# Performance work log

Hardware: AMD Instinct MI355X
Metric: run time of the kernel (lower is better)

## Reference

```python
import jax, jax.numpy as jnp
import numpy as np

K_PRED = 6
SCORE_TEMP = 0.5
MPA_THRESH = (2.5, 1.0, 2.0)   # meters, [veh, ped, cyc]
MTR_THRESH = (2.5, 1.0, 2.0)
TRACK_FUTURE = 91 - 11          # step_gt - step_current = 80


def setup_inputs() -> dict:
    key = jax.random.key(0)
    k1, k2, k3 = jax.random.split(key, 3)
    n_sc, n_ag, n_jf, n_step = 64, 64, 32, 80
    # scale 2.0 so endpoint pair distances straddle the ~2.5m NMS thresholds
    trajs = jax.random.normal(k1, (n_sc, n_jf, n_ag, n_step, 3), dtype=jnp.float32) * 2.0
    scores = jax.random.normal(k2, (n_sc, n_jf, n_ag), dtype=jnp.float32)
    ag_idx = jax.random.randint(k3, (n_sc, n_ag), 0, 3)
    ag_type = jax.nn.one_hot(ag_idx, 3, dtype=jnp.float32)  # [n_sc, n_ag, 3] one-hot
    return {"ag_type": ag_type, "trajs": trajs, "scores": scores}


def _type_thresh(ag_type, thresh_list):
    # ag_type [S,A,3] one-hot -> per-agent threshold [S,A]
    return ag_type @ jnp.asarray(thresh_list, dtype=ag_type.dtype)


def _endpoint_within(trajs, thresh):
    # use_ade=False: pairwise distance of final-step xy. trajs [S,A,J,T,3]
    end_xy = trajs[:, :, :, -1, :2]  # [S,A,J,2]
    d = jnp.linalg.norm(end_xy[:, :, :, None, :] - end_xy[:, :, None, :, :], axis=-1)
    return d < thresh[:, :, None, None]  # [S,A,J,J] bool


def _mtr_nms(trajs, scores, within, k_pred):
    # greedy: pick argmax, down-weight nearby modes by 0.01, kill picked with -1
    def step(sc, _):
        idx = jnp.argmax(sc, axis=-1)  # [S,A]
        w = jnp.take_along_axis(within, idx[:, :, None, None], axis=2)[:, :, 0]  # [S,A,J]
        sc = sc * ((~w).astype(sc.dtype) * 0.99 + 0.01)
        sc = jnp.where(jax.nn.one_hot(idx, sc.shape[-1], dtype=bool), -1.0, sc)
        return sc, idx

    _, idxs = jax.lax.scan(step, scores, None, length=k_pred)
    mode_idx = jnp.moveaxis(idxs, 0, -1)  # [S,A,k_pred]
    trajs_k = jnp.take_along_axis(trajs, mode_idx[:, :, :, None, None], axis=2)
    scores_k = jnp.take_along_axis(scores, mode_idx, axis=2)
    return trajs_k, scores_k / scores_k.sum(-1, keepdims=True)


def _mpa_nms_agent(scores, within):
    # scores [K], within [K,K]; visit modes in descending original-score order,
    # suppress mode k to 0.001 if any currently-higher-scoring mode is within thresh.
    order = jnp.argsort(-scores)

    def step(sc, k):
        mask = within[k] & (sc > sc[k])
        return sc.at[k].set(jnp.where(mask.any(), 0.001, sc[k])), None

    sc, _ = jax.lax.scan(step, scores, order)
    return sc


def reference(ag_type, trajs, scores):
    trajs = jnp.swapaxes(trajs, 1, 2)  # [S,A,J,T,3]
    scores = jax.nn.softmax(jnp.swapaxes(scores, 1, 2), axis=-1)  # [S,A,J]

    # mtr_nms: reduce n_joint_future -> k_pred (mtr_nms_thresh non-empty, aggr empty)
    within = _endpoint_within(trajs, _type_thresh(ag_type, MTR_THRESH))
    trajs, scores = _mtr_nms(trajs, scores, within, K_PRED)

    # mpa_nms: rescore the k_pred modes
    within = _endpoint_within(trajs, _type_thresh(ag_type, MPA_THRESH))
    scores = jax.vmap(jax.vmap(_mpa_nms_agent))(scores, within)
    scores = scores / scores.sum(-1, keepdims=True)

    # score temperature > 0
    scores = jax.nn.softmax(jnp.log(scores) / SCORE_TEMP, axis=-1)

    # downsample to 2Hz: [S,A,k_pred,16,3]
    return trajs[:, :, :, 4:TRACK_FUTURE:5], scores
```

## Files before the change

kernel.cpp:

```cpp
#include <hip/hip_runtime.h>


#define NSC 64
#define NAG 64
#define NJF 32
#define NSTEP 80
#define KP 6
#define TOUT 16

struct F3 { float x, y, z; };

__global__ __launch_bounds__(64)
void womd_pp2(const float* __restrict__ ag_type,
              const float* __restrict__ trajs,
              const float* __restrict__ scores,
              float* __restrict__ out)
{
    const int tid  = threadIdx.x;
    const int half = tid >> 5;
    const int hl   = tid & 31;
    const int s    = blockIdx.x >> 5;
    const int p    = blockIdx.x & 31;
    const int a    = p * 2 + half;

    __shared__ float exs[2][NJF][2];
    __shared__ float sms[2][NJF];
    __shared__ int   selsh[2][KP];

    float raw = scores[((size_t)s * NJF + hl) * NAG + a];
    size_t eoff = (((size_t)(s * NJF + hl) * NAG + a) * NSTEP + (NSTEP - 1)) * 3;
    float exx = trajs[eoff];
    float exy = trajs[eoff + 1];
    const float* at = ag_type + (size_t)(s * NAG + a) * 3;
    const float thresh = at[0] * 2.5f + at[1] * 1.0f + at[2] * 2.0f;

    exs[half][hl][0] = exx;
    exs[half][hl][1] = exy;

    float mx = raw;
    #pragma unroll
    for (int off = 16; off > 0; off >>= 1)
        mx = fmaxf(mx, __shfl_xor(mx, off, 32));
    float ev = expf(raw - mx);
    float sum = ev;
    #pragma unroll
    for (int off = 16; off > 0; off >>= 1)
        sum += __shfl_xor(sum, off, 32);
    float sm = ev / sum;
    sms[half][hl] = sm;

    __syncthreads();

    unsigned m = 0;
    #pragma unroll 8
    for (int j = 0; j < NJF; ++j) {
        float dx = exx - exs[half][j][0];
        float dy = exy - exs[half][j][1];
        if (sqrtf(dx * dx + dy * dy) < thresh) m |= (1u << j);
    }

    float ls = sm;
    #pragma unroll
    for (int k = 0; k < KP; ++k) {
        float v = ls; int idx = hl;
        #pragma unroll
        for (int off = 16; off > 0; off >>= 1) {
            float ov = __shfl_xor(v, off, 32);
            int   oi = __shfl_xor(idx, off, 32);
            if (ov > v || (ov == v && oi < idx)) { v = ov; idx = oi; }
        }
        unsigned wb = __shfl(m, idx, 32);
        ls *= ((wb >> hl) & 1u) ? 0.01f : 1.0f;
        if (hl == idx) ls = -1.0f;
        if (hl == 0) selsh[half][k] = idx;
    }
    __syncthreads();

    F3 pt[3];
    #pragma unroll
    for (int i = 0; i < 3; ++i) {
        int e  = hl + 32 * i;
        int mm = e >> 4;
        int t  = e & 15;
        int sj = selsh[half][mm];
        size_t src = (((size_t)(s * NJF + sj) * NAG + a) * NSTEP + (4 + 5 * t)) * 3;
        pt[i] = *(const F3*)(trajs + src);
    }

    if (hl == 0) {
        int   sel[KP];
        float sk[KP], sx[KP], sy[KP];
        float ssum = 0.f;
        #pragma unroll
        for (int k = 0; k < KP; ++k) {
            sel[k] = selsh[half][k];
            sk[k]  = sms[half][sel[k]];
            ssum  += sk[k];
            sx[k]  = exs[half][sel[k]][0];
            sy[k]  = exs[half][sel[k]][1];
        }
        #pragma unroll
        for (int k = 0; k < KP; ++k) sk[k] /= ssum;

        bool w2[KP][KP];
        #pragma unroll
        for (int i = 0; i < KP; ++i)
            #pragma unroll
            for (int j = 0; j < KP; ++j) {
                float dx = sx[i] - sx[j], dy = sy[i] - sy[j];
                w2[i][j] = sqrtf(dx * dx + dy * dy) < thresh;
            }

        int order[KP]; bool used[KP] = {false,false,false,false,false,false};
        #pragma unroll
        for (int t = 0; t < KP; ++t) {
            int best = -1; float bv = 0.f;
            #pragma unroll
            for (int j = 0; j < KP; ++j)
                if (!used[j] && (best < 0 || sk[j] > bv)) { best = j; bv = sk[j]; }
            order[t] = best; used[best] = true;
        }
        #pragma unroll
        for (int t = 0; t < KP; ++t) {
            int k = order[t];
            bool any = false;
            #pragma unroll
            for (int j = 0; j < KP; ++j)
                if (w2[k][j] && sk[j] > sk[k]) any = true;
            if (any) sk[k] = 0.001f;
        }

        float s2 = 0.f;
        #pragma unroll
        for (int k = 0; k < KP; ++k) s2 += sk[k];
        #pragma unroll
        for (int k = 0; k < KP; ++k) sk[k] /= s2;
        float s3 = 0.f; float q[KP];
        #pragma unroll
        for (int k = 0; k < KP; ++k) { q[k] = sk[k] * sk[k]; s3 += q[k]; }

        const size_t SCBASE = (size_t)NSC * NAG * KP * TOUT * 3;
        size_t scb = SCBASE + ((size_t)s * NAG + a) * KP;
        #pragma unroll
        for (int k = 0; k < KP; ++k) out[scb + k] = q[k] / s3;
    }

    size_t ob = ((size_t)s * NAG + a) * (KP * TOUT * 3);
    #pragma unroll
    for (int i = 0; i < 3; ++i) {
        int e = hl + 32 * i;
        *(F3*)(out + ob + (size_t)e * 3) = pt[i];
    }
}

extern "C" void kernel_launch(void* const* d_in, const int* in_sizes, int n_in,
                              void* d_out, int out_size, void* d_ws, size_t ws_size,
                              hipStream_t stream) {
    const float* ag_type = (const float*)d_in[0];
    const float* trajs   = (const float*)d_in[1];
    const float* scores  = (const float*)d_in[2];
    float* out = (float*)d_out;

    womd_pp2<<<NSC * (NAG / 2), 64, 0, stream>>>(ag_type, trajs, scores, out);
}
```

Before: 32.98 us.

## Parallelize MPA NMS across lanes and drop second block barrier

```diff
diff --git a/kernel.cpp b/kernel.cpp
--- a/kernel.cpp
+++ b/kernel.cpp
@@ -11,7 +11,7 @@
 struct F3 { float x, y, z; };
 
 __global__ __launch_bounds__(64)
-void womd_pp2(const float* __restrict__ ag_type,
+void womd_pp3(const float* __restrict__ ag_type,
               const float* __restrict__ trajs,
               const float* __restrict__ scores,
               float* __restrict__ out)
@@ -24,8 +24,6 @@
     const int a    = p * 2 + half;
 
     __shared__ float exs[2][NJF][2];
-    __shared__ float sms[2][NJF];
-    __shared__ int   selsh[2][KP];
 
     float raw = scores[((size_t)s * NJF + hl) * NAG + a];
     size_t eoff = (((size_t)(s * NJF + hl) * NAG + a) * NSTEP + (NSTEP - 1)) * 3;
@@ -47,18 +45,18 @@
     for (int off = 16; off > 0; off >>= 1)
         sum += __shfl_xor(sum, off, 32);
     float sm = ev / sum;
-    sms[half][hl] = sm;
 
     __syncthreads();
 
     unsigned m = 0;
-    #pragma unroll 8
+    #pragma unroll
     for (int j = 0; j < NJF; ++j) {
         float dx = exx - exs[half][j][0];
         float dy = exy - exs[half][j][1];
-        if (sqrtf(dx * dx + dy * dy) < thresh) m |= (1u << j);
+        m |= (sqrtf(dx * dx + dy * dy) < thresh) ? (1u << j) : 0u;
     }
 
+    int sel[KP];
     float ls = sm;
     #pragma unroll
     for (int k = 0; k < KP; ++k) {
@@ -67,89 +65,86 @@
         for (int off = 16; off > 0; off >>= 1) {
             float ov = __shfl_xor(v, off, 32);
             int   oi = __shfl_xor(idx, off, 32);
-            if (ov > v || (ov == v && oi < idx)) { v = ov; idx = oi; }
+            bool take = (ov > v) || (ov == v && oi < idx);
+            v   = take ? ov : v;
+            idx = take ? oi : idx;
         }
+        sel[k] = idx;
         unsigned wb = __shfl(m, idx, 32);
         ls *= ((wb >> hl) & 1u) ? 0.01f : 1.0f;
-        if (hl == idx) ls = -1.0f;
-        if (hl == 0) selsh[half][k] = idx;
+        ls = (hl == idx) ? -1.0f : ls;
     }
-    __syncthreads();
 
     F3 pt[3];
     #pragma unroll
     for (int i = 0; i < 3; ++i) {
-        int e  = hl + 32 * i;
-        int mm = e >> 4;
-        int t  = e & 15;
-        int sj = selsh[half][mm];
-        size_t src = (((size_t)(s * NJF + sj) * NAG + a) * NSTEP + (4 + 5 * t)) * 3;
+        int mode = (hl < 16) ? sel[2 * i] : sel[2 * i + 1];
+        int t = hl & 15;
+        size_t src = (((size_t)(s * NJF + mode) * NAG + a) * NSTEP + (4 + 5 * t)) * 3;
         pt[i] = *(const F3*)(trajs + src);
     }
 
-    if (hl == 0) {
-        int   sel[KP];
-        float sk[KP], sx[KP], sy[KP];
-        float ssum = 0.f;
-        #pragma unroll
-        for (int k = 0; k < KP; ++k) {
-            sel[k] = selsh[half][k];
-            sk[k]  = sms[half][sel[k]];
-            ssum  += sk[k];
-            sx[k]  = exs[half][sel[k]][0];
-            sy[k]  = exs[half][sel[k]][1];
-        }
-        #pragma unroll
-        for (int k = 0; k < KP; ++k) sk[k] /= ssum;
+    const bool active = (hl < KP);
+    int mySel = sel[0];
+    mySel = (hl == 1) ? sel[1] : mySel;
+    mySel = (hl == 2) ? sel[2] : mySel;
+    mySel = (hl == 3) ? sel[3] : mySel;
+    mySel = (hl == 4) ? sel[4] : mySel;
+    mySel = (hl == 5) ? sel[5] : mySel;
 
-        bool w2[KP][KP];
-        #pragma unroll
-        for (int i = 0; i < KP; ++i)
-            #pragma unroll
-            for (int j = 0; j < KP; ++j) {
-                float dx = sx[i] - sx[j], dy = sy[i] - sy[j];
-                w2[i][j] = sqrtf(dx * dx + dy * dy) < thresh;
-            }
+    float mySk = __shfl(sm, mySel, 32);
+    float myX  = __shfl(exx, mySel, 32);
+    float myY  = __shfl(exy, mySel, 32);
 
-        int order[KP]; bool used[KP] = {false,false,false,false,false,false};
-        #pragma unroll
-        for (int t = 0; t < KP; ++t) {
-            int best = -1; float bv = 0.f;
-            #pragma unroll
-            for (int j = 0; j < KP; ++j)
-                if (!used[j] && (best < 0 || sk[j] > bv)) { best = j; bv = sk[j]; }
-            order[t] = best; used[best] = true;
-        }
-        #pragma unroll
-        for (int t = 0; t < KP; ++t) {
-            int k = order[t];
-            bool any = false;
-            #pragma unroll
-            for (int j = 0; j < KP; ++j)
-                if (w2[k][j] && sk[j] > sk[k]) any = true;
-            if (any) sk[k] = 0.001f;
-        }
+    float t0 = active ? mySk : 0.f;
+    t0 += __shfl_xor(t0, 4, 8);
+    t0 += __shfl_xor(t0, 2, 8);
+    t0 += __shfl_xor(t0, 1, 8);
+    float skn = mySk / t0;
 
-        float s2 = 0.f;
-        #pragma unroll
-        for (int k = 0; k < KP; ++k) s2 += sk[k];
-        #pragma unroll
-        for (int k = 0; k < KP; ++k) sk[k] /= s2;
-        float s3 = 0.f; float q[KP];
-        #pragma unroll
-        for (int k = 0; k < KP; ++k) { q[k] = sk[k] * sk[k]; s3 += q[k]; }
+    unsigned w2row = 0;
+    int rank = 0;
+    #pragma unroll
+    for (int jj = 0; jj < KP; ++jj) {
+        float ox  = __shfl(myX, jj, 32);
+        float oy  = __shfl(myY, jj, 32);
+        float osk = __shfl(skn, jj, 32);
+        float dx = myX - ox, dy = myY - oy;
+        if (sqrtf(dx * dx + dy * dy) < thresh) w2row |= (1u << jj);
+        rank += ((osk > skn) || (osk == skn && jj < hl)) ? 1 : 0;
+    }
+    if (!active) rank = 99;
 
-        const size_t SCBASE = (size_t)NSC * NAG * KP * TOUT * 3;
-        size_t scb = SCBASE + ((size_t)s * NAG + a) * KP;
-        #pragma unroll
-        for (int k = 0; k < KP; ++k) out[scb + k] = q[k] / s3;
+    #pragma unroll
+    for (int t = 0; t < KP; ++t) {
+        unsigned long long bal = __ballot(rank == t);
+        unsigned bits = half ? (unsigned)(bal >> 32) : (unsigned)bal;
+        int kk = __ffs(bits) - 1;
+        float sk_k = __shfl(skn, kk, 32);
+        bool cond = active && ((w2row >> kk) & 1u) && (skn > sk_k);
+        unsigned long long b2 = __ballot(cond);
+        unsigned hb = half ? (unsigned)(b2 >> 32) : (unsigned)b2;
+        if (hb != 0 && hl == kk) skn = 0.001f;
     }
+
+    float t1 = active ? skn : 0.f;
+    t1 += __shfl_xor(t1, 4, 8);
+    t1 += __shfl_xor(t1, 2, 8);
+    t1 += __shfl_xor(t1, 1, 8);
+    float pn = skn / t1;
+    float q = pn * pn;
+    float t2 = active ? q : 0.f;
+    t2 += __shfl_xor(t2, 4, 8);
+    t2 += __shfl_xor(t2, 2, 8);
+    t2 += __shfl_xor(t2, 1, 8);
+
+    const size_t SCBASE = (size_t)NSC * NAG * KP * TOUT * 3;
+    if (active) out[SCBASE + ((size_t)s * NAG + a) * KP + hl] = q / t2;
 
     size_t ob = ((size_t)s * NAG + a) * (KP * TOUT * 3);
     #pragma unroll
     for (int i = 0; i < 3; ++i) {
-        int e = hl + 32 * i;
-        *(F3*)(out + ob + (size_t)e * 3) = pt[i];
+        *(F3*)(out + ob + (size_t)(hl + 32 * i) * 3) = pt[i];
     }
 }
 
@@ -161,5 +156,5 @@
     const float* scores  = (const float*)d_in[2];
     float* out = (float*)d_out;
 
-    womd_pp2<<<NSC * (NAG / 2), 64, 0, stream>>>(ag_type, trajs, scores, out);
+    womd_pp3<<<NSC * (NAG / 2), 64, 0, stream>>>(ag_type, trajs, scores, out);
 }
```

After: 40.79 us. +23.7%, slower.

## Split trajectory gather into a separate kernel via workspace index buffer

Applied to the files above, without the earlier changes.

```diff
diff --git a/kernel.cpp b/kernel.cpp
--- a/kernel.cpp
+++ b/kernel.cpp
@@ -11,10 +11,11 @@
 struct F3 { float x, y, z; };
 
 __global__ __launch_bounds__(64)
-void womd_pp2(const float* __restrict__ ag_type,
+void womd_sel(const float* __restrict__ ag_type,
               const float* __restrict__ trajs,
               const float* __restrict__ scores,
-              float* __restrict__ out)
+              float* __restrict__ out,
+              int* __restrict__ selbase)
 {
     const int tid  = threadIdx.x;
     const int half = tid >> 5;
@@ -25,7 +26,6 @@
 
     __shared__ float exs[2][NJF][2];
     __shared__ float sms[2][NJF];
-    __shared__ int   selsh[2][KP];
 
     float raw = scores[((size_t)s * NJF + hl) * NAG + a];
     size_t eoff = (((size_t)(s * NJF + hl) * NAG + a) * NSTEP + (NSTEP - 1)) * 3;
@@ -59,6 +59,7 @@
         if (sqrtf(dx * dx + dy * dy) < thresh) m |= (1u << j);
     }
 
+    int sel[KP];
     float ls = sm;
     #pragma unroll
     for (int k = 0; k < KP; ++k) {
@@ -72,28 +73,14 @@
         unsigned wb = __shfl(m, idx, 32);
         ls *= ((wb >> hl) & 1u) ? 0.01f : 1.0f;
         if (hl == idx) ls = -1.0f;
-        if (hl == 0) selsh[half][k] = idx;
-    }
-    __syncthreads();
-
-    F3 pt[3];
-    #pragma unroll
-    for (int i = 0; i < 3; ++i) {
-        int e  = hl + 32 * i;
-        int mm = e >> 4;
-        int t  = e & 15;
-        int sj = selsh[half][mm];
-        size_t src = (((size_t)(s * NJF + sj) * NAG + a) * NSTEP + (4 + 5 * t)) * 3;
-        pt[i] = *(const F3*)(trajs + src);
+        sel[k] = idx;
     }
 
     if (hl == 0) {
-        int   sel[KP];
         float sk[KP], sx[KP], sy[KP];
         float ssum = 0.f;
         #pragma unroll
         for (int k = 0; k < KP; ++k) {
-            sel[k] = selsh[half][k];
             sk[k]  = sms[half][sel[k]];
             ssum  += sk[k];
             sx[k]  = exs[half][sel[k]][0];
@@ -143,14 +130,25 @@
         size_t scb = SCBASE + ((size_t)s * NAG + a) * KP;
         #pragma unroll
         for (int k = 0; k < KP; ++k) out[scb + k] = q[k] / s3;
+
+        int bm = (s * NAG + a) * KP;
+        #pragma unroll
+        for (int k = 0; k < KP; ++k)
+            selbase[bm + k] = ((s * NJF + sel[k]) * NAG + a) * (NSTEP * 3);
     }
+}
 
-    size_t ob = ((size_t)s * NAG + a) * (KP * TOUT * 3);
-    #pragma unroll
-    for (int i = 0; i < 3; ++i) {
-        int e = hl + 32 * i;
-        *(F3*)(out + ob + (size_t)e * 3) = pt[i];
-    }
+__global__ __launch_bounds__(256)
+void womd_gather(const float* __restrict__ trajs,
+                 const int* __restrict__ selbase,
+                 float* __restrict__ out)
+{
+    int e  = blockIdx.x * 256 + threadIdx.x;
+    int t  = e & 15;
+    int bm = e >> 4;
+    int base = selbase[bm];
+    F3 v = *(const F3*)(trajs + (size_t)base + (size_t)(4 + 5 * t) * 3);
+    *(F3*)(out + (size_t)e * 3) = v;
 }
 
 extern "C" void kernel_launch(void* const* d_in, const int* in_sizes, int n_in,
@@ -160,6 +158,10 @@
     const float* trajs   = (const float*)d_in[1];
     const float* scores  = (const float*)d_in[2];
     float* out = (float*)d_out;
+    int* selbase = (int*)d_ws;
 
-    womd_pp2<<<NSC * (NAG / 2), 64, 0, stream>>>(ag_type, trajs, scores, out);
+    womd_sel<<<NSC * (NAG / 2), 64, 0, stream>>>(ag_type, trajs, scores, out, selbase);
+
+    const int total = NSC * NAG * KP * TOUT;
+    womd_gather<<<total / 256, 256, 0, stream>>>(trajs, selbase, out);
 }
```

New measurement: 41.65 us. 26.3% more time.

## Assign one agent per block and spread trajectory gather over all 64 lanes

Applied to the files above, without the earlier changes.

```diff
diff --git a/kernel.cpp b/kernel.cpp
--- a/kernel.cpp
+++ b/kernel.cpp
@@ -11,21 +11,20 @@
 struct F3 { float x, y, z; };
 
 __global__ __launch_bounds__(64)
-void womd_pp2(const float* __restrict__ ag_type,
+void womd_pp7(const float* __restrict__ ag_type,
               const float* __restrict__ trajs,
               const float* __restrict__ scores,
               float* __restrict__ out)
 {
-    const int tid  = threadIdx.x;
-    const int half = tid >> 5;
-    const int hl   = tid & 31;
-    const int s    = blockIdx.x >> 5;
-    const int p    = blockIdx.x & 31;
-    const int a    = p * 2 + half;
+    const int tid = threadIdx.x;
+    const int hl  = tid & 31;
+    const int b   = blockIdx.x;
+    const int s   = b >> 6;
+    const int a   = b & 63;
 
-    __shared__ float exs[2][NJF][2];
-    __shared__ float sms[2][NJF];
-    __shared__ int   selsh[2][KP];
+    __shared__ float exs[NJF][2];
+    __shared__ float sms[NJF];
+    __shared__ int   selsh[KP];
 
     float raw = scores[((size_t)s * NJF + hl) * NAG + a];
     size_t eoff = (((size_t)(s * NJF + hl) * NAG + a) * NSTEP + (NSTEP - 1)) * 3;
@@ -34,8 +33,10 @@
     const float* at = ag_type + (size_t)(s * NAG + a) * 3;
     const float thresh = at[0] * 2.5f + at[1] * 1.0f + at[2] * 2.0f;
 
-    exs[half][hl][0] = exx;
-    exs[half][hl][1] = exy;
+    if (tid < NJF) {
+        exs[hl][0] = exx;
+        exs[hl][1] = exy;
+    }
 
     float mx = raw;
     #pragma unroll
@@ -47,15 +48,15 @@
     for (int off = 16; off > 0; off >>= 1)
         sum += __shfl_xor(sum, off, 32);
     float sm = ev / sum;
-    sms[half][hl] = sm;
+    if (tid < NJF) sms[hl] = sm;
 
     __syncthreads();
 
     unsigned m = 0;
     #pragma unroll 8
     for (int j = 0; j < NJF; ++j) {
-        float dx = exx - exs[half][j][0];
-        float dy = exy - exs[half][j][1];
+        float dx = exx - exs[j][0];
+        float dy = exy - exs[j][1];
         if (sqrtf(dx * dx + dy * dy) < thresh) m |= (1u << j);
     }
 
@@ -72,32 +73,38 @@
         unsigned wb = __shfl(m, idx, 32);
         ls *= ((wb >> hl) & 1u) ? 0.01f : 1.0f;
         if (hl == idx) ls = -1.0f;
-        if (hl == 0) selsh[half][k] = idx;
+        if (tid == 0) selsh[k] = idx;
     }
     __syncthreads();
 
-    F3 pt[3];
-    #pragma unroll
-    for (int i = 0; i < 3; ++i) {
-        int e  = hl + 32 * i;
+    F3 pt0, pt1;
+    {
+        int mm = tid >> 4;
+        int t  = tid & 15;
+        int sj = selsh[mm];
+        size_t src = (((size_t)(s * NJF + sj) * NAG + a) * NSTEP + (4 + 5 * t)) * 3;
+        pt0 = *(const F3*)(trajs + src);
+    }
+    if (tid < 32) {
+        int e  = 64 + tid;
         int mm = e >> 4;
         int t  = e & 15;
-        int sj = selsh[half][mm];
+        int sj = selsh[mm];
         size_t src = (((size_t)(s * NJF + sj) * NAG + a) * NSTEP + (4 + 5 * t)) * 3;
-        pt[i] = *(const F3*)(trajs + src);
+        pt1 = *(const F3*)(trajs + src);
     }
 
-    if (hl == 0) {
+    if (tid == 0) {
         int   sel[KP];
         float sk[KP], sx[KP], sy[KP];
         float ssum = 0.f;
         #pragma unroll
         for (int k = 0; k < KP; ++k) {
-            sel[k] = selsh[half][k];
-            sk[k]  = sms[half][sel[k]];
+            sel[k] = selsh[k];
+            sk[k]  = sms[sel[k]];
             ssum  += sk[k];
-            sx[k]  = exs[half][sel[k]][0];
-            sy[k]  = exs[half][sel[k]][1];
+            sx[k]  = exs[sel[k]][0];
+            sy[k]  = exs[sel[k]][1];
         }
         #pragma unroll
         for (int k = 0; k < KP; ++k) sk[k] /= ssum;
@@ -146,11 +153,9 @@
     }
 
     size_t ob = ((size_t)s * NAG + a) * (KP * TOUT * 3);
-    #pragma unroll
-    for (int i = 0; i < 3; ++i) {
-        int e = hl + 32 * i;
-        *(F3*)(out + ob + (size_t)e * 3) = pt[i];
-    }
+    *(F3*)(out + ob + (size_t)tid * 3) = pt0;
+    if (tid < 32)
+        *(F3*)(out + ob + (size_t)(64 + tid) * 3) = pt1;
 }
 
 extern "C" void kernel_launch(void* const* d_in, const int* in_sizes, int n_in,
@@ -161,5 +166,5 @@
     const float* scores  = (const float*)d_in[2];
     float* out = (float*)d_out;
 
-    womd_pp2<<<NSC * (NAG / 2), 64, 0, stream>>>(ag_type, trajs, scores, out);
+    womd_pp7<<<NSC * NAG, 64, 0, stream>>>(ag_type, trajs, scores, out);
 }
```

After: 66.58 us. 102% more time.
